# Optimization experiments

Measured on AMD Instinct MI355X. Metric: run time of the kernel, lower is better.

## Reference

```python
import jax, jax.numpy as jnp
import numpy as np

B, R = 4096, 2048

def setup_inputs() -> dict:
    key = jax.random.key(0)
    twist_batch = jax.random.normal(key, (B, R, 3), dtype=jnp.float32)
    return {"twist_batch": twist_batch}

def _rodrigues(twist_batch):
    # twist_batch: [B, R, 3]
    # rot_angle: clamp(||w||, 1e-5)
    rot_angle = jnp.maximum(jnp.linalg.norm(twist_batch, axis=2, keepdims=True), 1e-5)  # [B,R,1]
    axis = twist_batch / rot_angle  # [B,R,3]
    a0, a1, a2 = axis[..., 0], axis[..., 1], axis[..., 2]
    o = jnp.zeros_like(a0)
    # skew-symmetric cross-product matrix A: [B,R,3,3]
    A = jnp.stack([o, -a2, a1,
                   a2, o, -a0,
                   -a1, a0, o], axis=-1).reshape(*a0.shape, 3, 3)
    s = jnp.sin(rot_angle)[..., None]          # [B,R,1,1]
    c1 = (1.0 - jnp.cos(rot_angle))[..., None]  # [B,R,1,1]
    AA = jnp.matmul(A, A)                       # batched 3x3 mm
    I = jnp.eye(3, dtype=twist_batch.dtype)
    return I + A * s + AA * c1  # [B,R,3,3]

def reference(twist_batch):
    return _rodrigues(twist_batch)
```

## Files before the change

### kernel.cpp

```cpp
#include <hip/hip_runtime.h>
#include <math.h>


#define TPB 256

__global__ __launch_bounds__(TPB) void twist2mat_kernel(
    const float* __restrict__ in, float* __restrict__ out) {
    const int tid = threadIdx.x;
    const int base_in  = blockIdx.x * (3 * TPB);
    const int base_out = blockIdx.x * (9 * TPB);

    __shared__ float si[3 * TPB];
    __shared__ float so[9 * TPB];

    si[tid]            = in[base_in + tid];
    si[tid + TPB]      = in[base_in + tid + TPB];
    si[tid + 2 * TPB]  = in[base_in + tid + 2 * TPB];
    __syncthreads();

    const float w0 = si[3 * tid + 0];
    const float w1 = si[3 * tid + 1];
    const float w2 = si[3 * tid + 2];

    const float n2  = fmaf(w0, w0, fmaf(w1, w1, w2 * w2));
    const float t   = fmaxf(sqrtf(n2), 1e-5f);
    const float inv = 1.0f / t;
    const float a0 = w0 * inv, a1 = w1 * inv, a2 = w2 * inv;

    float s, c;
    __sincosf(t, &s, &c);
    const float c1 = 1.0f - c;

    const float aa = fmaf(a0, a0, fmaf(a1, a1, a2 * a2));

    float* r = &so[9 * tid];
    r[0] = fmaf(c1, fmaf(a0, a0, -aa), 1.0f);
    r[1] = fmaf(c1, a0 * a1, -s * a2);
    r[2] = fmaf(c1, a0 * a2,  s * a1);
    r[3] = fmaf(c1, a0 * a1,  s * a2);
    r[4] = fmaf(c1, fmaf(a1, a1, -aa), 1.0f);
    r[5] = fmaf(c1, a1 * a2, -s * a0);
    r[6] = fmaf(c1, a0 * a2, -s * a1);
    r[7] = fmaf(c1, a1 * a2,  s * a0);
    r[8] = fmaf(c1, fmaf(a2, a2, -aa), 1.0f);
    __syncthreads();

#pragma unroll
    for (int k = 0; k < 9; ++k)
        out[base_out + tid + TPB * k] = so[tid + TPB * k];
}

extern "C" void kernel_launch(void* const* d_in, const int* in_sizes, int n_in,
                              void* d_out, int out_size, void* d_ws, size_t ws_size,
                              hipStream_t stream) {
    (void)n_in; (void)out_size; (void)d_ws; (void)ws_size;
    const float* in = (const float*)d_in[0];
    float* out = (float*)d_out;
    const int nrot = in_sizes[0] / 3;
    const int grid = nrot / TPB;
    twist2mat_kernel<<<grid, TPB, 0, stream>>>(in, out);
}
```

Measured before the change: 363.4 us.

## Process four rotations per thread with float4 vectorized nontemporal loads and stores

Each thread now handles four rotations. Input and output move as 128-bit vectors through one shared staging buffer, and the global loads and stores use nontemporal hints. This cuts the number of memory instructions and blocks for a purely bandwidth-bound elementwise kernel. In exchange, register pressure rises from the 36-float output array, and the 16-byte strided LDS accesses may cause bank conflicts.

```diff
diff --git a/kernel.cpp b/kernel.cpp
--- a/kernel.cpp
+++ b/kernel.cpp
@@ -2,61 +2,79 @@
 #include <math.h>
 
 
+typedef float v4f __attribute__((ext_vector_type(4)));
+
 #define TPB 256
+#define RPT 4
+#define RPB (TPB * RPT)
+#define IN_F4 (RPB * 3 / 4)
+#define OUT_F4 (RPB * 9 / 4)
 
 __global__ __launch_bounds__(TPB) void twist2mat_kernel(
-    const float* __restrict__ in, float* __restrict__ out) {
+    const v4f* __restrict__ in4, v4f* __restrict__ out4) {
     const int tid = threadIdx.x;
-    const int base_in  = blockIdx.x * (3 * TPB);
-    const int base_out = blockIdx.x * (9 * TPB);
+    const int bin  = blockIdx.x * IN_F4;
+    const int bout = blockIdx.x * OUT_F4;
 
-    __shared__ float si[3 * TPB];
-    __shared__ float so[9 * TPB];
+    __shared__ v4f buf[OUT_F4];
 
-    si[tid]            = in[base_in + tid];
-    si[tid + TPB]      = in[base_in + tid + TPB];
-    si[tid + 2 * TPB]  = in[base_in + tid + 2 * TPB];
+#pragma unroll
+    for (int k = 0; k < 3; ++k)
+        buf[tid + TPB * k] = __builtin_nontemporal_load(&in4[bin + tid + TPB * k]);
     __syncthreads();
 
-    const float w0 = si[3 * tid + 0];
-    const float w1 = si[3 * tid + 1];
-    const float w2 = si[3 * tid + 2];
+    const v4f x0 = buf[3 * tid + 0];
+    const v4f x1 = buf[3 * tid + 1];
+    const v4f x2 = buf[3 * tid + 2];
+    __syncthreads();
 
-    const float n2  = fmaf(w0, w0, fmaf(w1, w1, w2 * w2));
-    const float t   = fmaxf(sqrtf(n2), 1e-5f);
-    const float inv = 1.0f / t;
-    const float a0 = w0 * inv, a1 = w1 * inv, a2 = w2 * inv;
+    const float w[12] = {x0.x, x0.y, x0.z, x0.w,
+                         x1.x, x1.y, x1.z, x1.w,
+                         x2.x, x2.y, x2.z, x2.w};
+    float o[36];
+#pragma unroll
+    for (int j = 0; j < 4; ++j) {
+        const float w0 = w[3 * j], w1 = w[3 * j + 1], w2 = w[3 * j + 2];
+        const float n2  = fmaf(w0, w0, fmaf(w1, w1, w2 * w2));
+        const float t   = fmaxf(sqrtf(n2), 1e-5f);
+        const float inv = 1.0f / t;
+        const float a0 = w0 * inv, a1 = w1 * inv, a2 = w2 * inv;
+        float s, c;
+        __sincosf(t, &s, &c);
+        const float c1 = 1.0f - c;
+        const float aa = fmaf(a0, a0, fmaf(a1, a1, a2 * a2));
+        float* r = &o[9 * j];
+        r[0] = fmaf(c1, fmaf(a0, a0, -aa), 1.0f);
+        r[1] = fmaf(c1, a0 * a1, -s * a2);
+        r[2] = fmaf(c1, a0 * a2,  s * a1);
+        r[3] = fmaf(c1, a0 * a1,  s * a2);
+        r[4] = fmaf(c1, fmaf(a1, a1, -aa), 1.0f);
+        r[5] = fmaf(c1, a1 * a2, -s * a0);
+        r[6] = fmaf(c1, a0 * a2, -s * a1);
+        r[7] = fmaf(c1, a1 * a2,  s * a0);
+        r[8] = fmaf(c1, fmaf(a2, a2, -aa), 1.0f);
+    }
 
-    float s, c;
-    __sincosf(t, &s, &c);
-    const float c1 = 1.0f - c;
-
-    const float aa = fmaf(a0, a0, fmaf(a1, a1, a2 * a2));
-
-    float* r = &so[9 * tid];
-    r[0] = fmaf(c1, fmaf(a0, a0, -aa), 1.0f);
-    r[1] = fmaf(c1, a0 * a1, -s * a2);
-    r[2] = fmaf(c1, a0 * a2,  s * a1);
-    r[3] = fmaf(c1, a0 * a1,  s * a2);
-    r[4] = fmaf(c1, fmaf(a1, a1, -aa), 1.0f);
-    r[5] = fmaf(c1, a1 * a2, -s * a0);
-    r[6] = fmaf(c1, a0 * a2, -s * a1);
-    r[7] = fmaf(c1, a1 * a2,  s * a0);
-    r[8] = fmaf(c1, fmaf(a2, a2, -aa), 1.0f);
+#pragma unroll
+    for (int k = 0; k < 9; ++k) {
+        v4f v = {o[4 * k + 0], o[4 * k + 1], o[4 * k + 2], o[4 * k + 3]};
+        buf[9 * tid + k] = v;
+    }
     __syncthreads();
 
 #pragma unroll
     for (int k = 0; k < 9; ++k)
-        out[base_out + tid + TPB * k] = so[tid + TPB * k];
+        __builtin_nontemporal_store(buf[tid + TPB * k],
+                                    &out4[bout + tid + TPB * k]);
 }
 
 extern "C" void kernel_launch(void* const* d_in, const int* in_sizes, int n_in,
                               void* d_out, int out_size, void* d_ws, size_t ws_size,
                               hipStream_t stream) {
     (void)n_in; (void)out_size; (void)d_ws; (void)ws_size;
-    const float* in = (const float*)d_in[0];
-    float* out = (float*)d_out;
+    const v4f* in4 = (const v4f*)d_in[0];
+    v4f* out4 = (v4f*)d_out;
     const int nrot = in_sizes[0] / 3;
-    const int grid = nrot / TPB;
-    twist2mat_kernel<<<grid, TPB, 0, stream>>>(in, out);
+    const int grid = nrot / RPB;
+    twist2mat_kernel<<<grid, TPB, 0, stream>>>(in4, out4);
 }
```

Result: faster. 353.6 us (-2.7%).
